# Kernel optimization log

Hardware: AMD Instinct MI355X
Metric: run time of the kernel (lower is better)

The kernel has to match this reference:

```python
import jax, jax.numpy as jnp
import numpy as np

EPS = 1e-5

def layernorm(x, gamma, beta):
    # torch.var default is unbiased (ddof=1) - faithful to source
    m = jnp.mean(x, axis=-1, keepdims=True)
    d = x.shape[-1]
    var = jnp.sum((x - m) ** 2, axis=-1, keepdims=True) / (d - 1)
    return gamma * (x - m) / jnp.sqrt(var + EPS) + beta

def setup_inputs() -> dict:
    key = jax.random.key(0)
    B, S, D, H = 8, 1024, 768, 12
    hd = D // H
    ks = jax.random.split(key, 20)
    s_in = 1.0 / np.sqrt(D)
    s_ff = 1.0 / np.sqrt(4 * D)
    return {
        "x":  jax.random.normal(ks[0], (B, S, D), jnp.float32),
        "Wq": jax.random.uniform(ks[1], (H, D, hd), jnp.float32, -s_in, s_in),
        "bq": jax.random.uniform(ks[2], (H, hd), jnp.float32, -s_in, s_in),
        "Wk": jax.random.uniform(ks[3], (H, D, hd), jnp.float32, -s_in, s_in),
        "bk": jax.random.uniform(ks[4], (H, hd), jnp.float32, -s_in, s_in),
        "Wv": jax.random.uniform(ks[5], (H, D, hd), jnp.float32, -s_in, s_in),
        "bv": jax.random.uniform(ks[6], (H, hd), jnp.float32, -s_in, s_in),
        "Wo": jax.random.uniform(ks[7], (D, D), jnp.float32, -s_in, s_in),
        "bo": jax.random.uniform(ks[8], (D,), jnp.float32, -s_in, s_in),
        "W1": jax.random.uniform(ks[9], (D, 4 * D), jnp.float32, -s_in, s_in),
        "b1": jax.random.uniform(ks[10], (4 * D,), jnp.float32, -s_in, s_in),
        "W2": jax.random.uniform(ks[11], (4 * D, D), jnp.float32, -s_ff, s_ff),
        "b2": jax.random.uniform(ks[12], (D,), jnp.float32, -s_ff, s_ff),
        "g1": jnp.ones((D,), jnp.float32),
        "be1": jnp.zeros((D,), jnp.float32),
        "g2": jnp.ones((D,), jnp.float32),
        "be2": jnp.zeros((D,), jnp.float32),
    }

def reference(x, Wq, bq, Wk, bk, Wv, bv, Wo, bo, W1, b1, W2, b2, g1, be1, g2, be2):
    # x = ln1(x); x = x + mha(x); x = ln2(x); out = x + ffwd(x)
    x = layernorm(x, g1, be1)
    hd = Wq.shape[-1]
    q = jnp.einsum('bsd,hdk->bhsk', x, Wq) + bq[None, :, None, :]
    k = jnp.einsum('bsd,hdk->bhsk', x, Wk) + bk[None, :, None, :]
    v = jnp.einsum('bsd,hdk->bhsk', x, Wv) + bv[None, :, None, :]
    att = jnp.einsum('bhqk,bhsk->bhqs', q, k) * (hd ** -0.5)
    att = jax.nn.softmax(att, axis=-1)
    o = jnp.einsum('bhqs,bhsk->bhqk', att, v)  # [B,H,S,hd]
    B, H, S, _ = o.shape
    o = jnp.transpose(o, (0, 2, 1, 3)).reshape(B, S, H * hd)  # concat heads
    x = x + o @ Wo + bo
    x = layernorm(x, g2, be2)
    h = jax.nn.gelu(x @ W1 + b1, approximate=False)
    out = x + h @ W2 + b2
    return out
```

## Files before the change

kernel.cpp:

```cpp
#include <hip/hip_runtime.h>
#include <stdint.h>

typedef __attribute__((ext_vector_type(8))) short bf16x8;
typedef __attribute__((ext_vector_type(4))) float f32x4;

#define GPTR(p) ((const __attribute__((address_space(1))) void*)(p))
#define LPTR(p) ((__attribute__((address_space(3))) void*)(p))

__device__ __forceinline__ float b2f(unsigned short u) {
  union { unsigned int i; float f; } v; v.i = ((unsigned int)u) << 16; return v.f;
}
__device__ __forceinline__ unsigned short f2b(float f) {
  union { float f; unsigned int i; } v; v.f = f;
  unsigned int i = v.i;
  return (unsigned short)((i + 0x7FFFu + ((i >> 16) & 1u)) >> 16);
}

template <int FP32IN>
__global__ __launch_bounds__(256) void ln_kernel(const void* __restrict__ xin,
                                                 const float* __restrict__ g,
                                                 const float* __restrict__ be,
                                                 unsigned short* __restrict__ y) {
  const int D = 768;
  int row = blockIdx.x;
  int t = threadIdx.x;
  float v[3];
  float s = 0.f, s2 = 0.f;
#pragma unroll
  for (int i = 0; i < 3; ++i) {
    int c = t + i * 256;
    float f;
    if (FP32IN) f = ((const float*)xin)[(size_t)row * D + c];
    else        f = b2f(((const unsigned short*)xin)[(size_t)row * D + c]);
    v[i] = f; s += f; s2 += f * f;
  }
#pragma unroll
  for (int d = 32; d > 0; d >>= 1) { s += __shfl_down(s, d); s2 += __shfl_down(s2, d); }
  __shared__ float red[8];
  int w = t >> 6;
  if ((t & 63) == 0) { red[w] = s; red[4 + w] = s2; }
  __syncthreads();
  s = red[0] + red[1] + red[2] + red[3];
  s2 = red[4] + red[5] + red[6] + red[7];
  float mean = s * (1.0f / 768.0f);
  float var = (s2 - 768.0f * mean * mean) * (1.0f / 767.0f);
  float rstd = rsqrtf(var + 1e-5f);
  unsigned short* yr = y + (size_t)row * D;
#pragma unroll
  for (int i = 0; i < 3; ++i) {
    int c = t + i * 256;
    yr[c] = f2b((v[i] - mean) * rstd * g[c] + be[c]);
  }
}

__global__ __launch_bounds__(256) void castT_kernel(const float* __restrict__ in,
                                                    unsigned short* __restrict__ out,
                                                    int R, int C, long in_z, long out_z) {
  __shared__ float tile[32][33];
  long z = blockIdx.z;
  in += z * in_z; out += z * out_z;
  int c0 = blockIdx.x * 32, r0 = blockIdx.y * 32;
  int tc = threadIdx.x & 31, tr = threadIdx.x >> 5;
#pragma unroll
  for (int i = 0; i < 4; ++i) {
    int r = tr + i * 8;
    tile[r][tc] = in[(size_t)(r0 + r) * C + c0 + tc];
  }
  __syncthreads();
#pragma unroll
  for (int i = 0; i < 4; ++i) {
    int r = tr + i * 8;
    out[(size_t)(c0 + r) * R + r0 + tc] = f2b(tile[tc][r]);
  }
}

template <int EPI>
__global__ __launch_bounds__(256) void gemm_bt(const unsigned short* __restrict__ A,
                                               const unsigned short* __restrict__ Bt,
                                               int M, int N, int K,
                                               const float* __restrict__ bias0,
                                               const float* __restrict__ bias1,
                                               const float* __restrict__ bias2,
                                               const unsigned short* __restrict__ res,
                                               unsigned short* __restrict__ out0,
                                               unsigned short* __restrict__ out1,
                                               unsigned short* __restrict__ out2,
                                               float* __restrict__ outf) {
  __shared__ unsigned short As[128 * 32];
  __shared__ unsigned short Bs[128 * 32];
  int t = threadIdx.x;
  int n0 = blockIdx.x * 128, m0 = blockIdx.y * 128;
  int lane = t & 63, w = t >> 6;
  int lr = lane & 15, quad = lane >> 4;
  int wm = (w >> 1) * 64, wn = (w & 1) * 64;
  int rowInWave = lane >> 2;
  int colq = (lane & 3) * 8;
  f32x4 zero4 = {0.f, 0.f, 0.f, 0.f};
  f32x4 acc[4][4];
#pragma unroll
  for (int i = 0; i < 4; ++i)
#pragma unroll
    for (int j = 0; j < 4; ++j) acc[i][j] = zero4;
  for (int k0 = 0; k0 < K; k0 += 32) {
    __syncthreads();
#pragma unroll
    for (int rnd = 0; rnd < 2; ++rnd) {
      int rbase = rnd * 64 + w * 16;
      int row = rbase + rowInWave;
      __builtin_amdgcn_global_load_lds(GPTR(A + (size_t)(m0 + row) * K + k0 + colq),
                                       LPTR(&As[rbase * 32]), 16, 0, 0);
      __builtin_amdgcn_global_load_lds(GPTR(Bt + (size_t)(n0 + row) * K + k0 + colq),
                                       LPTR(&Bs[rbase * 32]), 16, 0, 0);
    }
    __syncthreads();
    bf16x8 af[4];
#pragma unroll
    for (int i = 0; i < 4; ++i)
      af[i] = *(const bf16x8*)(&As[(wm + i * 16 + lr) * 32 + quad * 8]);
#pragma unroll
    for (int j = 0; j < 4; ++j) {
      bf16x8 bfr = *(const bf16x8*)(&Bs[(wn + j * 16 + lr) * 32 + quad * 8]);
#pragma unroll
      for (int i = 0; i < 4; ++i)
        acc[i][j] = __builtin_amdgcn_mfma_f32_16x16x32_bf16(af[i], bfr, acc[i][j], 0, 0, 0);
    }
  }
#pragma unroll
  for (int i = 0; i < 4; ++i) {
#pragma unroll
    for (int j = 0; j < 4; ++j) {
#pragma unroll
      for (int r = 0; r < 4; ++r) {
        int rg = m0 + wm + i * 16 + quad * 4 + r;
        int cg = n0 + wn + j * 16 + lr;
        float val = acc[i][j][r];
        if (EPI == 1) {
          int b = rg >> 10, sx = rg & 1023;
          if (cg < 768) {
            int h = cg >> 6, kk = cg & 63;
            out0[(((size_t)(b * 12 + h) << 10) + sx) * 64 + kk] = f2b(val + bias0[cg]);
          } else if (cg < 1536) {
            int cc = cg - 768, h = cc >> 6, kk = cc & 63;
            out1[(((size_t)(b * 12 + h) << 10) + sx) * 64 + kk] = f2b(val + bias1[cc]);
          } else {
            int cc = cg - 1536, h = cc >> 6, kk = cc & 63;
            out2[((size_t)(b * 12 + h) << 16) + ((size_t)kk << 10) + sx] = f2b(val + bias2[cc]);
          }
        } else if (EPI == 2) {
          val += bias0[cg] + b2f(res[(size_t)rg * N + cg]);
          out0[(size_t)rg * N + cg] = f2b(val);
        } else if (EPI == 3) {
          float xg = val + bias0[cg];
          val = 0.5f * xg * (1.0f + erff(xg * 0.70710678118654752f));
          out0[(size_t)rg * N + cg] = f2b(val);
        } else if (EPI == 4) {
          outf[(size_t)rg * N + cg] = val + bias0[cg] + b2f(res[(size_t)rg * N + cg]);
        }
      }
    }
  }
}

__global__ __launch_bounds__(256) void attn_kernel(const unsigned short* __restrict__ q,
                                                   const unsigned short* __restrict__ k,
                                                   const unsigned short* __restrict__ vt,
                                                   unsigned short* __restrict__ out) {
  __shared__ unsigned short Ks[64 * 72];
  __shared__ unsigned short Vs[64 * 72];
  __shared__ unsigned short Ps[4][32 * 72];
  int bh = blockIdx.y;
  int q0 = blockIdx.x * 128;
  int t = threadIdx.x, lane = t & 63, w = t >> 6;
  int lr = lane & 15, quad = lane >> 4;
  const unsigned short* qb = q + (size_t)bh * 1024 * 64;
  const unsigned short* kb = k + (size_t)bh * 1024 * 64;
  const unsigned short* vb = vt + (size_t)bh * 64 * 1024;
  bf16x8 aq[2][2];
#pragma unroll
  for (int i = 0; i < 2; ++i)
#pragma unroll
    for (int ks = 0; ks < 2; ++ks)
      aq[i][ks] = *(const bf16x8*)(qb + (size_t)(q0 + w * 32 + i * 16 + lr) * 64 + ks * 32 + quad * 8);
  f32x4 zero4 = {0.f, 0.f, 0.f, 0.f};
  f32x4 oacc[2][4];
  float l_part[2][4];
#pragma unroll
  for (int i = 0; i < 2; ++i)
#pragma unroll
    for (int j = 0; j < 4; ++j) oacc[i][j] = zero4;
#pragma unroll
  for (int i = 0; i < 2; ++i)
#pragma unroll
    for (int r = 0; r < 4; ++r) l_part[i][r] = 0.f;
  int srow = t >> 3, spart = t & 7;
  unsigned short* ps = &Ps[w][0];
  for (int st = 0; st < 16; ++st) {
    int s0 = st * 64;
    __syncthreads();
#pragma unroll
    for (int rnd = 0; rnd < 2; ++rnd) {
      int rr = rnd * 32 + srow;
      *(uint4*)(&Ks[rr * 72 + spart * 8]) = *(const uint4*)(kb + (size_t)(s0 + rr) * 64 + spart * 8);
      *(uint4*)(&Vs[rr * 72 + spart * 8]) = *(const uint4*)(vb + (size_t)rr * 1024 + s0 + spart * 8);
    }
    __syncthreads();
#pragma unroll
    for (int i = 0; i < 2; ++i) {
#pragma unroll
      for (int j = 0; j < 4; ++j) {
        bf16x8 bk0 = *(const bf16x8*)(&Ks[(j * 16 + lr) * 72 + quad * 8]);
        bf16x8 bk1 = *(const bf16x8*)(&Ks[(j * 16 + lr) * 72 + 32 + quad * 8]);
        f32x4 z = zero4;
        z = __builtin_amdgcn_mfma_f32_16x16x32_bf16(aq[i][0], bk0, z, 0, 0, 0);
        z = __builtin_amdgcn_mfma_f32_16x16x32_bf16(aq[i][1], bk1, z, 0, 0, 0);
#pragma unroll
        for (int r = 0; r < 4; ++r) {
          float p = __expf(z[r] * 0.125f);
          l_part[i][r] += p;
          ps[(i * 16 + quad * 4 + r) * 72 + j * 16 + lr] = f2b(p);
        }
      }
    }
    __syncthreads();
#pragma unroll
    for (int i = 0; i < 2; ++i) {
#pragma unroll
      for (int ks = 0; ks < 2; ++ks) {
        bf16x8 ap = *(const bf16x8*)(&ps[(i * 16 + lr) * 72 + ks * 32 + quad * 8]);
#pragma unroll
        for (int j = 0; j < 4; ++j) {
          bf16x8 bv = *(const bf16x8*)(&Vs[(j * 16 + lr) * 72 + ks * 32 + quad * 8]);
          oacc[i][j] = __builtin_amdgcn_mfma_f32_16x16x32_bf16(ap, bv, oacc[i][j], 0, 0, 0);
        }
      }
    }
  }
  int b = bh / 12, h = bh % 12;
#pragma unroll
  for (int i = 0; i < 2; ++i) {
#pragma unroll
    for (int r = 0; r < 4; ++r) {
      float l = l_part[i][r];
#pragma unroll
      for (int d = 1; d < 16; d <<= 1) l += __shfl_xor(l, d);
      float inv = 1.0f / l;
      int sx = q0 + w * 32 + i * 16 + quad * 4 + r;
      size_t base = ((size_t)(b * 1024 + sx)) * 768 + h * 64;
#pragma unroll
      for (int j = 0; j < 4; ++j)
        out[base + j * 16 + lr] = f2b(oacc[i][j][r] * inv);
    }
  }
}

extern "C" void kernel_launch(void* const* d_in, const int* in_sizes, int n_in,
                              void* d_out, int out_size, void* d_ws, size_t ws_size,
                              hipStream_t stream) {
  const float* x  = (const float*)d_in[0];
  const float* Wq = (const float*)d_in[1];
  const float* bq = (const float*)d_in[2];
  const float* Wk = (const float*)d_in[3];
  const float* bk = (const float*)d_in[4];
  const float* Wv = (const float*)d_in[5];
  const float* bv = (const float*)d_in[6];
  const float* Wo = (const float*)d_in[7];
  const float* bo = (const float*)d_in[8];
  const float* W1 = (const float*)d_in[9];
  const float* b1 = (const float*)d_in[10];
  const float* W2 = (const float*)d_in[11];
  const float* b2 = (const float*)d_in[12];
  const float* g1 = (const float*)d_in[13];
  const float* be1= (const float*)d_in[14];
  const float* g2 = (const float*)d_in[15];
  const float* be2= (const float*)d_in[16];
  float* outf = (float*)d_out;

  const size_t SLOT = (size_t)8192 * 768;
  unsigned short* ws = (unsigned short*)d_ws;
  unsigned short* Wqkvt = ws;
  unsigned short* Wot   = Wqkvt + (size_t)2304 * 768;
  unsigned short* W1t   = Wot   + (size_t)768 * 768;
  unsigned short* W2t   = W1t   + (size_t)3072 * 768;
  unsigned short* s0    = W2t   + (size_t)768 * 3072;
  unsigned short* s1    = s0 + SLOT;
  unsigned short* s2    = s1 + SLOT;
  unsigned short* s3    = s2 + SLOT;
  unsigned short* s4    = s3 + SLOT;

  unsigned short* qbuf = s0;
  unsigned short* kbuf = s1;
  unsigned short* y    = s2;
  unsigned short* x2   = s3;
  unsigned short* ao   = s4;
  unsigned short* y2   = s4;
  unsigned short* hb   = s0;
  unsigned short* vtb  = (unsigned short*)d_out;

  castT_kernel<<<dim3(2, 24, 12), 256, 0, stream>>>(Wq, Wqkvt,              768, 64, 768 * 64, 64 * 768);
  castT_kernel<<<dim3(2, 24, 12), 256, 0, stream>>>(Wk, Wqkvt + 768 * 768,  768, 64, 768 * 64, 64 * 768);
  castT_kernel<<<dim3(2, 24, 12), 256, 0, stream>>>(Wv, Wqkvt + 1536 * 768, 768, 64, 768 * 64, 64 * 768);
  castT_kernel<<<dim3(24, 24, 1), 256, 0, stream>>>(Wo, Wot, 768, 768, 0, 0);
  castT_kernel<<<dim3(96, 24, 1), 256, 0, stream>>>(W1, W1t, 768, 3072, 0, 0);
  castT_kernel<<<dim3(24, 96, 1), 256, 0, stream>>>(W2, W2t, 3072, 768, 0, 0);

  ln_kernel<1><<<8192, 256, 0, stream>>>(x, g1, be1, y);
  gemm_bt<1><<<dim3(18, 64), 256, 0, stream>>>(y, Wqkvt, 8192, 2304, 768,
                                               bq, bk, bv, nullptr, qbuf, kbuf, vtb, nullptr);
  attn_kernel<<<dim3(8, 96), 256, 0, stream>>>(qbuf, kbuf, vtb, ao);
  gemm_bt<2><<<dim3(6, 64), 256, 0, stream>>>(ao, Wot, 8192, 768, 768,
                                              bo, nullptr, nullptr, y, x2, nullptr, nullptr, nullptr);
  ln_kernel<0><<<8192, 256, 0, stream>>>(x2, g2, be2, y2);
  gemm_bt<3><<<dim3(24, 64), 256, 0, stream>>>(y2, W1t, 8192, 3072, 768,
                                               b1, nullptr, nullptr, nullptr, hb, nullptr, nullptr, nullptr);
  gemm_bt<4><<<dim3(6, 64), 256, 0, stream>>>(hb, W2t, 8192, 768, 3072,
                                              b2, nullptr, nullptr, y2, nullptr, nullptr, nullptr, outf);
}
```

Before: 455.6 us.

## Merge weight cast/transpose and first layernorm into one launch; deepen GEMM K step

The six weight cast-transpose launches and the first layernorm are folded into a single prep kernel that picks its role from the block index, removing six kernel launches and the gaps between them. The GEMM main loop now stages two 32-wide K slices per barrier pair (a 64-wide K step), halving the number of __syncthreads per tile. This doubles LDS use per GEMM block, which may lower occupancy, and there is still no overlap between loads and compute.

```diff
diff --git a/kernel.cpp b/kernel.cpp
--- a/kernel.cpp
+++ b/kernel.cpp
@@ -16,8 +16,7 @@
   return (unsigned short)((i + 0x7FFFu + ((i >> 16) & 1u)) >> 16);
 }
 
-template <int FP32IN>
-__global__ __launch_bounds__(256) void ln_kernel(const void* __restrict__ xin,
+__global__ __launch_bounds__(256) void ln_kernel(const unsigned short* __restrict__ xin,
                                                  const float* __restrict__ g,
                                                  const float* __restrict__ be,
                                                  unsigned short* __restrict__ y) {
@@ -29,9 +28,7 @@
 #pragma unroll
   for (int i = 0; i < 3; ++i) {
     int c = t + i * 256;
-    float f;
-    if (FP32IN) f = ((const float*)xin)[(size_t)row * D + c];
-    else        f = b2f(((const unsigned short*)xin)[(size_t)row * D + c]);
+    float f = b2f(xin[(size_t)row * D + c]);
     v[i] = f; s += f; s2 += f * f;
   }
 #pragma unroll
@@ -53,24 +50,81 @@
   }
 }
 
-__global__ __launch_bounds__(256) void castT_kernel(const float* __restrict__ in,
-                                                    unsigned short* __restrict__ out,
-                                                    int R, int C, long in_z, long out_z) {
-  __shared__ float tile[32][33];
-  long z = blockIdx.z;
-  in += z * in_z; out += z * out_z;
-  int c0 = blockIdx.x * 32, r0 = blockIdx.y * 32;
-  int tc = threadIdx.x & 31, tr = threadIdx.x >> 5;
-#pragma unroll
-  for (int i = 0; i < 4; ++i) {
-    int r = tr + i * 8;
-    tile[r][tc] = in[(size_t)(r0 + r) * C + c0 + tc];
-  }
-  __syncthreads();
-#pragma unroll
-  for (int i = 0; i < 4; ++i) {
-    int r = tr + i * 8;
-    out[(size_t)(c0 + r) * R + r0 + tc] = f2b(tile[tc][r]);
+__global__ __launch_bounds__(256) void prep_kernel(const float* __restrict__ Wq,
+                                                   const float* __restrict__ Wk,
+                                                   const float* __restrict__ Wv,
+                                                   const float* __restrict__ Wo,
+                                                   const float* __restrict__ W1,
+                                                   const float* __restrict__ W2,
+                                                   const float* __restrict__ x,
+                                                   const float* __restrict__ g1,
+                                                   const float* __restrict__ be1,
+                                                   unsigned short* __restrict__ Wqkvt,
+                                                   unsigned short* __restrict__ Wot,
+                                                   unsigned short* __restrict__ W1t,
+                                                   unsigned short* __restrict__ W2t,
+                                                   unsigned short* __restrict__ y) {
+  int bid = blockIdx.x;
+  int t = threadIdx.x;
+  if (bid < 6912) {
+    __shared__ float tile[32][33];
+    const float* in; unsigned short* out; int R, C, c0, r0;
+    if (bid < 1728) {
+      int seg = bid / 576, r = bid % 576;
+      int z = r / 48, t2 = r % 48, bx = t2 & 1, by = t2 >> 1;
+      in = (seg == 0 ? Wq : seg == 1 ? Wk : Wv) + (size_t)z * 768 * 64;
+      out = Wqkvt + (size_t)seg * 768 * 768 + (size_t)z * 64 * 768;
+      R = 768; C = 64; c0 = bx * 32; r0 = by * 32;
+    } else if (bid < 2304) {
+      int r = bid - 1728, bx = r % 24, by = r / 24;
+      in = Wo; out = Wot; R = 768; C = 768; c0 = bx * 32; r0 = by * 32;
+    } else if (bid < 4608) {
+      int r = bid - 2304, bx = r % 96, by = r / 96;
+      in = W1; out = W1t; R = 768; C = 3072; c0 = bx * 32; r0 = by * 32;
+    } else {
+      int r = bid - 4608, bx = r % 24, by = r / 24;
+      in = W2; out = W2t; R = 3072; C = 768; c0 = bx * 32; r0 = by * 32;
+    }
+    int tc = t & 31, tr = t >> 5;
+#pragma unroll
+    for (int i = 0; i < 4; ++i) {
+      int r = tr + i * 8;
+      tile[r][tc] = in[(size_t)(r0 + r) * C + c0 + tc];
+    }
+    __syncthreads();
+#pragma unroll
+    for (int i = 0; i < 4; ++i) {
+      int r = tr + i * 8;
+      out[(size_t)(c0 + r) * R + r0 + tc] = f2b(tile[tc][r]);
+    }
+  } else {
+    const int D = 768;
+    int row = bid - 6912;
+    float v[3];
+    float s = 0.f, s2 = 0.f;
+#pragma unroll
+    for (int i = 0; i < 3; ++i) {
+      int c = t + i * 256;
+      float f = x[(size_t)row * D + c];
+      v[i] = f; s += f; s2 += f * f;
+    }
+#pragma unroll
+    for (int d = 32; d > 0; d >>= 1) { s += __shfl_down(s, d); s2 += __shfl_down(s2, d); }
+    __shared__ float red[8];
+    int w = t >> 6;
+    if ((t & 63) == 0) { red[w] = s; red[4 + w] = s2; }
+    __syncthreads();
+    s = red[0] + red[1] + red[2] + red[3];
+    s2 = red[4] + red[5] + red[6] + red[7];
+    float mean = s * (1.0f / 768.0f);
+    float var = (s2 - 768.0f * mean * mean) * (1.0f / 767.0f);
+    float rstd = rsqrtf(var + 1e-5f);
+    unsigned short* yr = y + (size_t)row * D;
+#pragma unroll
+    for (int i = 0; i < 3; ++i) {
+      int c = t + i * 256;
+      yr[c] = f2b((v[i] - mean) * rstd * g1[c] + be1[c]);
+    }
   }
 }
 
@@ -86,8 +140,8 @@
                                                unsigned short* __restrict__ out1,
                                                unsigned short* __restrict__ out2,
                                                float* __restrict__ outf) {
-  __shared__ unsigned short As[128 * 32];
-  __shared__ unsigned short Bs[128 * 32];
+  __shared__ unsigned short As[2][128 * 32];
+  __shared__ unsigned short Bs[2][128 * 32];
   int t = threadIdx.x;
   int n0 = blockIdx.x * 128, m0 = blockIdx.y * 128;
   int lane = t & 63, w = t >> 6;
@@ -101,28 +155,34 @@
   for (int i = 0; i < 4; ++i)
 #pragma unroll
     for (int j = 0; j < 4; ++j) acc[i][j] = zero4;
-  for (int k0 = 0; k0 < K; k0 += 32) {
-    __syncthreads();
-#pragma unroll
-    for (int rnd = 0; rnd < 2; ++rnd) {
-      int rbase = rnd * 64 + w * 16;
-      int row = rbase + rowInWave;
-      __builtin_amdgcn_global_load_lds(GPTR(A + (size_t)(m0 + row) * K + k0 + colq),
-                                       LPTR(&As[rbase * 32]), 16, 0, 0);
-      __builtin_amdgcn_global_load_lds(GPTR(Bt + (size_t)(n0 + row) * K + k0 + colq),
-                                       LPTR(&Bs[rbase * 32]), 16, 0, 0);
-    }
-    __syncthreads();
-    bf16x8 af[4];
-#pragma unroll
-    for (int i = 0; i < 4; ++i)
-      af[i] = *(const bf16x8*)(&As[(wm + i * 16 + lr) * 32 + quad * 8]);
-#pragma unroll
-    for (int j = 0; j < 4; ++j) {
-      bf16x8 bfr = *(const bf16x8*)(&Bs[(wn + j * 16 + lr) * 32 + quad * 8]);
+  for (int k0 = 0; k0 < K; k0 += 64) {
+    __syncthreads();
+#pragma unroll
+    for (int s = 0; s < 2; ++s) {
+#pragma unroll
+      for (int rnd = 0; rnd < 2; ++rnd) {
+        int rbase = rnd * 64 + w * 16;
+        int row = rbase + rowInWave;
+        __builtin_amdgcn_global_load_lds(GPTR(A + (size_t)(m0 + row) * K + k0 + s * 32 + colq),
+                                         LPTR(&As[s][rbase * 32]), 16, 0, 0);
+        __builtin_amdgcn_global_load_lds(GPTR(Bt + (size_t)(n0 + row) * K + k0 + s * 32 + colq),
+                                         LPTR(&Bs[s][rbase * 32]), 16, 0, 0);
+      }
+    }
+    __syncthreads();
+#pragma unroll
+    for (int s = 0; s < 2; ++s) {
+      bf16x8 af[4];
 #pragma unroll
       for (int i = 0; i < 4; ++i)
-        acc[i][j] = __builtin_amdgcn_mfma_f32_16x16x32_bf16(af[i], bfr, acc[i][j], 0, 0, 0);
+        af[i] = *(const bf16x8*)(&As[s][(wm + i * 16 + lr) * 32 + quad * 8]);
+#pragma unroll
+      for (int j = 0; j < 4; ++j) {
+        bf16x8 bfr = *(const bf16x8*)(&Bs[s][(wn + j * 16 + lr) * 32 + quad * 8]);
+#pragma unroll
+        for (int i = 0; i < 4; ++i)
+          acc[i][j] = __builtin_amdgcn_mfma_f32_16x16x32_bf16(af[i], bfr, acc[i][j], 0, 0, 0);
+      }
     }
   }
 #pragma unroll
@@ -296,20 +356,15 @@
   unsigned short* hb   = s0;
   unsigned short* vtb  = (unsigned short*)d_out;
 
-  castT_kernel<<<dim3(2, 24, 12), 256, 0, stream>>>(Wq, Wqkvt,              768, 64, 768 * 64, 64 * 768);
-  castT_kernel<<<dim3(2, 24, 12), 256, 0, stream>>>(Wk, Wqkvt + 768 * 768,  768, 64, 768 * 64, 64 * 768);
-  castT_kernel<<<dim3(2, 24, 12), 256, 0, stream>>>(Wv, Wqkvt + 1536 * 768, 768, 64, 768 * 64, 64 * 768);
-  castT_kernel<<<dim3(24, 24, 1), 256, 0, stream>>>(Wo, Wot, 768, 768, 0, 0);
-  castT_kernel<<<dim3(96, 24, 1), 256, 0, stream>>>(W1, W1t, 768, 3072, 0, 0);
-  castT_kernel<<<dim3(24, 96, 1), 256, 0, stream>>>(W2, W2t, 3072, 768, 0, 0);
-
-  ln_kernel<1><<<8192, 256, 0, stream>>>(x, g1, be1, y);
+  prep_kernel<<<6912 + 8192, 256, 0, stream>>>(Wq, Wk, Wv, Wo, W1, W2, x, g1, be1,
+                                               Wqkvt, Wot, W1t, W2t, y);
+
   gemm_bt<1><<<dim3(18, 64), 256, 0, stream>>>(y, Wqkvt, 8192, 2304, 768,
                                                bq, bk, bv, nullptr, qbuf, kbuf, vtb, nullptr);
   attn_kernel<<<dim3(8, 96), 256, 0, stream>>>(qbuf, kbuf, vtb, ao);
   gemm_bt<2><<<dim3(6, 64), 256, 0, stream>>>(ao, Wot, 8192, 768, 768,
                                               bo, nullptr, nullptr, y, x2, nullptr, nullptr, nullptr);
-  ln_kernel<0><<<8192, 256, 0, stream>>>(x2, g2, be2, y2);
+  ln_kernel<<<8192, 256, 0, stream>>>(x2, g2, be2, y2);
   gemm_bt<3><<<dim3(24, 64), 256, 0, stream>>>(y2, W1t, 8192, 3072, 768,
                                                b1, nullptr, nullptr, nullptr, hb, nullptr, nullptr, nullptr);
   gemm_bt<4><<<dim3(6, 64), 256, 0, stream>>>(hb, W2t, 8192, 768, 3072,
```

New measurement: 443.6 us. -2.6%, faster.
